# Performance work log

Measured on AMD Instinct MI355X. Metric: run time of the kernel, lower is better.

Reference implementation:

```python
import jax, jax.numpy as jnp
import numpy as np


def _conv(x, kernel):
    # x: [N, C, H, W], kernel: [O, I, kh, kw]; torch conv2d padding=1 (symmetric both dims)
    return jax.lax.conv_general_dilated(
        x, kernel, window_strides=(1, 1), padding=((1, 1), (1, 1)),
        dimension_numbers=("NCHW", "OIHW", "NCHW"))


def setup_inputs() -> dict:
    key = jax.random.key(0)
    k1, k2 = jax.random.split(key)
    shape = (2, 7, 7, 3, 256, 256)  # bs, ah, aw, c, h, w
    infer = jax.random.normal(k1, shape, dtype=jnp.float32)
    ref = jax.random.normal(k2, shape, dtype=jnp.float32)
    return {"infer": infer, "ref": ref}


def reference(infer, ref):
    bs, ah, aw, c, h, w = infer.shape
    x = infer.reshape(bs * ah * aw, c, h, w)
    y = ref.reshape(bs * ah * aw, c, h, w)
    # fixed gradient kernels, identical across all 3x3 in/out channel pairs
    kh = jnp.broadcast_to(
        jnp.array([-0.5, 0.0, 0.5], jnp.float32).reshape(1, 1, 1, 3), (3, 3, 1, 3))
    kv = jnp.broadcast_to(
        jnp.array([-0.5, 0.0, 0.5], jnp.float32).reshape(1, 1, 3, 1), (3, 3, 3, 1))
    # torch padding=1 on a (1,3) kernel -> output (h+2, w); on (3,1) -> (h, w+2)
    loss_h = jnp.mean(jnp.abs(_conv(x, kh) - _conv(y, kh)))
    loss_v = jnp.mean(jnp.abs(_conv(x, kv) - _conv(y, kv)))
    return (loss_h + loss_v) / 2.0
```

## Files before the change

kernel.cpp:

```cpp
#include <hip/hip_runtime.h>


#define W 256
#define NIMG 98
#define CH_STRIDE 65536
#define WAVES_PER_BLK 4
#define NROWS (NIMG * 256)
#define NBLK (NROWS / WAVES_PER_BLK)
#define NXCD 8
#define SCALE (0.25f / 6472704.0f)

struct Row6 { float4 a0, a1, a2, b0, b1, b2; };

__device__ __forceinline__ Row6 issue6(const float* __restrict__ xb,
                                       const float* __restrict__ yb, int ro) {
  Row6 r;
  r.a0 = *(const float4*)(xb + ro);
  r.a1 = *(const float4*)(xb + ro + CH_STRIDE);
  r.a2 = *(const float4*)(xb + ro + 2 * CH_STRIDE);
  r.b0 = *(const float4*)(yb + ro);
  r.b1 = *(const float4*)(yb + ro + CH_STRIDE);
  r.b2 = *(const float4*)(yb + ro + 2 * CH_STRIDE);
  return r;
}

__device__ __forceinline__ float4 combine(const Row6& r, float m) {
  float4 d;
  d.x = m * ((r.a0.x - r.b0.x) + (r.a1.x - r.b1.x) + (r.a2.x - r.b2.x));
  d.y = m * ((r.a0.y - r.b0.y) + (r.a1.y - r.b1.y) + (r.a2.y - r.b2.y));
  d.z = m * ((r.a0.z - r.b0.z) + (r.a1.z - r.b1.z) + (r.a2.z - r.b2.z));
  d.w = m * ((r.a0.w - r.b0.w) + (r.a1.w - r.b1.w) + (r.a2.w - r.b2.w));
  return d;
}

__device__ __forceinline__ float row_task(const float* __restrict__ x,
                                          const float* __restrict__ y,
                                          int task, int lane) {
  const int n = task >> 8;
  const int h = task & 255;

  const float* xb = x + (size_t)n * 3 * CH_STRIDE + (lane << 2);
  const float* yb = y + (size_t)n * 3 * CH_STRIDE + (lane << 2);

  const int hm = (h > 0)   ? h - 1 : 0;
  const int hp = (h < 255) ? h + 1 : 255;

  Row6 rm = issue6(xb, yb, hm * W);
  Row6 rc = issue6(xb, yb, h  * W);
  Row6 rp = issue6(xb, yb, hp * W);

  float4 dm = combine(rm, (h > 0)   ? 1.f : 0.f);
  float4 dc = combine(rc, 1.f);
  float4 dp = combine(rp, (h < 255) ? 1.f : 0.f);

  float lm = __shfl_up(dc.w, 1);
  if (lane == 0) lm = 0.f;
  float rr = __shfl_down(dc.x, 1);
  if (lane == 63) rr = 0.f;
  float acc = fabsf(dc.y - lm) + fabsf(dc.z - dc.x)
            + fabsf(dc.w - dc.y) + fabsf(rr - dc.z);

  acc += fabsf(dp.x - dm.x) + fabsf(dp.y - dm.y)
       + fabsf(dp.z - dm.z) + fabsf(dp.w - dm.w);

  #pragma unroll
  for (int off = 32; off > 0; off >>= 1)
    acc += __shfl_down(acc, off, 64);
  return acc;
}

__device__ __forceinline__ int swz_block(int bid) {
  const int chunk = NBLK / NXCD;
  return (bid % NXCD) * chunk + bid / NXCD;
}

__device__ __forceinline__ float block_body(const float* __restrict__ x,
                                            const float* __restrict__ y) {
  const int tid  = threadIdx.x;
  const int lane = tid & 63;
  const int wv   = tid >> 6;
  const int task = swz_block(blockIdx.x) * WAVES_PER_BLK + wv;

  float s = row_task(x, y, task, lane);

  __shared__ float ws[WAVES_PER_BLK];
  if (lane == 0) ws[wv] = s;
  __syncthreads();
  return ws[0] + ws[1] + ws[2] + ws[3];
}

__global__ __launch_bounds__(256) void detail_stage1(
    const float* __restrict__ x, const float* __restrict__ y,
    float* __restrict__ partial) {
  float s = block_body(x, y);
  if (threadIdx.x == 0) partial[blockIdx.x] = s;
}

__global__ __launch_bounds__(256) void detail_stage1_atomic(
    const float* __restrict__ x, const float* __restrict__ y,
    float* __restrict__ out) {
  float s = block_body(x, y);
  if (threadIdx.x == 0) atomicAdd(out, s * SCALE);
}

__global__ __launch_bounds__(256) void detail_stage2(
    const float* __restrict__ partial, float* __restrict__ out) {
  float acc = 0.f;
  for (int i = threadIdx.x; i < NBLK; i += 256) acc += partial[i];
  #pragma unroll
  for (int off = 32; off > 0; off >>= 1)
    acc += __shfl_down(acc, off, 64);
  __shared__ float ws[4];
  if ((threadIdx.x & 63) == 0) ws[threadIdx.x >> 6] = acc;
  __syncthreads();
  if (threadIdx.x == 0) out[0] = (ws[0] + ws[1] + ws[2] + ws[3]) * SCALE;
}

extern "C" void kernel_launch(void* const* d_in, const int* in_sizes, int n_in,
                              void* d_out, int out_size, void* d_ws, size_t ws_size,
                              hipStream_t stream) {
  const float* infer = (const float*)d_in[0];
  const float* ref   = (const float*)d_in[1];
  float* out = (float*)d_out;

  if (ws_size >= NBLK * sizeof(float)) {
    float* partial = (float*)d_ws;
    detail_stage1<<<NBLK, 256, 0, stream>>>(infer, ref, partial);
    detail_stage2<<<1, 256, 0, stream>>>(partial, out);
  } else {
    hipMemsetAsync(out, 0, sizeof(float), stream);
    detail_stage1_atomic<<<NBLK, 256, 0, stream>>>(infer, ref, out);
  }
}
```

Baseline: 180.5 us.

## Split into channel-difference pass plus stencil pass over materialized D buffer

Adds a first kernel that reduces the six input planes to a single difference image D, written to workspace, and a second kernel where each wave handles a 4-row strip of D, reusing loaded rows across neighbouring stencil rows instead of reloading three rows from six planes per output row. This removes the threefold redundant reads of the inputs that the old one-row-per-wave kernel relied on the cache to absorb. The cost is an extra round trip of D through global memory (about a third of the input size), an additional kernel launch, and the need for a much larger workspace. The old atomic fallback path is kept, but without XCD block swizzling.

```diff
diff --git a/kernel.cpp b/kernel.cpp
--- a/kernel.cpp
+++ b/kernel.cpp
@@ -4,11 +4,99 @@
 #define W 256
 #define NIMG 98
 #define CH_STRIDE 65536
-#define WAVES_PER_BLK 4
-#define NROWS (NIMG * 256)
-#define NBLK (NROWS / WAVES_PER_BLK)
-#define NXCD 8
+#define IMG_F4 16384
+#define TOT_F4 (NIMG * IMG_F4)
+#define P1_BLK (TOT_F4 / 256)
+#define NBAND2 (NIMG * 64)
+#define P2_BLK (NBAND2 / 4)
+#define D_FLOATS (NIMG * 65536)
+#define WS_NEED ((size_t)D_FLOATS * 4 + P2_BLK * 4)
 #define SCALE (0.25f / 6472704.0f)
+
+__global__ __launch_bounds__(256) void compute_d(
+    const float* __restrict__ x, const float* __restrict__ y,
+    float4* __restrict__ D) {
+  const int i = blockIdx.x * 256 + threadIdx.x;
+  const int n = i >> 14;
+  const int e = i & 16383;
+  const float4* xb = (const float4*)x + (size_t)n * 3 * IMG_F4 + e;
+  const float4* yb = (const float4*)y + (size_t)n * 3 * IMG_F4 + e;
+  const float4 a0 = xb[0], a1 = xb[IMG_F4], a2 = xb[2 * IMG_F4];
+  const float4 b0 = yb[0], b1 = yb[IMG_F4], b2 = yb[2 * IMG_F4];
+  float4 d;
+  d.x = (a0.x - b0.x) + (a1.x - b1.x) + (a2.x - b2.x);
+  d.y = (a0.y - b0.y) + (a1.y - b1.y) + (a2.y - b2.y);
+  d.z = (a0.z - b0.z) + (a1.z - b1.z) + (a2.z - b2.z);
+  d.w = (a0.w - b0.w) + (a1.w - b1.w) + (a2.w - b2.w);
+  D[i] = d;
+}
+
+__global__ __launch_bounds__(256) void detail_stencil(
+    const float4* __restrict__ D, float* __restrict__ partial) {
+  const int tid  = threadIdx.x;
+  const int lane = tid & 63;
+  const int wv   = tid >> 6;
+  const int band = blockIdx.x * 4 + wv;
+  const int n     = band >> 6;
+  const int strip = band & 63;
+  const int r0    = strip * 4;
+
+  const float4* Db = D + (size_t)n * IMG_F4 + lane;
+
+  const int gm = (r0 > 0) ? (r0 - 1) : 0;
+  const int gp = (r0 + 4 < 256) ? (r0 + 4) : 255;
+
+  float4 d0 = Db[gm * 64];
+  float4 d1 = Db[r0 * 64];
+  float4 d2 = Db[(r0 + 1) * 64];
+  float4 d3 = Db[(r0 + 2) * 64];
+  float4 d4 = Db[(r0 + 3) * 64];
+  float4 d5 = Db[gp * 64];
+
+  const float m0 = (r0 > 0) ? 1.f : 0.f;
+  const float m5 = (r0 + 4 < 256) ? 1.f : 0.f;
+  d0.x *= m0; d0.y *= m0; d0.z *= m0; d0.w *= m0;
+  d5.x *= m5; d5.y *= m5; d5.z *= m5; d5.w *= m5;
+
+  float acc = 0.f;
+  #define ACCROW(Dm, Dc, Dp) do {                                     \
+    float lm_ = __shfl_up((Dc).w, 1);                                 \
+    if (lane == 0) lm_ = 0.f;                                         \
+    float rr_ = __shfl_down((Dc).x, 1);                               \
+    if (lane == 63) rr_ = 0.f;                                        \
+    acc += fabsf((Dc).y - lm_) + fabsf((Dc).z - (Dc).x)              \
+         + fabsf((Dc).w - (Dc).y) + fabsf(rr_ - (Dc).z);             \
+    acc += fabsf((Dp).x - (Dm).x) + fabsf((Dp).y - (Dm).y)           \
+         + fabsf((Dp).z - (Dm).z) + fabsf((Dp).w - (Dm).w);          \
+  } while (0)
+
+  ACCROW(d0, d1, d2);
+  ACCROW(d1, d2, d3);
+  ACCROW(d2, d3, d4);
+  ACCROW(d3, d4, d5);
+  #undef ACCROW
+
+  #pragma unroll
+  for (int off = 32; off > 0; off >>= 1)
+    acc += __shfl_down(acc, off, 64);
+  __shared__ float ws[4];
+  if (lane == 0) ws[wv] = acc;
+  __syncthreads();
+  if (tid == 0) partial[blockIdx.x] = ws[0] + ws[1] + ws[2] + ws[3];
+}
+
+__global__ __launch_bounds__(256) void detail_stage2(
+    const float* __restrict__ partial, float* __restrict__ out) {
+  float acc = 0.f;
+  for (int i = threadIdx.x; i < P2_BLK; i += 256) acc += partial[i];
+  #pragma unroll
+  for (int off = 32; off > 0; off >>= 1)
+    acc += __shfl_down(acc, off, 64);
+  __shared__ float ws[4];
+  if ((threadIdx.x & 63) == 0) ws[threadIdx.x >> 6] = acc;
+  __syncthreads();
+  if (threadIdx.x == 0) out[0] = (ws[0] + ws[1] + ws[2] + ws[3]) * SCALE;
+}
 
 struct Row6 { float4 a0, a1, a2, b0, b1, b2; };
 
@@ -33,23 +121,25 @@
   return d;
 }
 
-__device__ __forceinline__ float row_task(const float* __restrict__ x,
-                                          const float* __restrict__ y,
-                                          int task, int lane) {
+__global__ __launch_bounds__(256) void detail_atomic(
+    const float* __restrict__ x, const float* __restrict__ y,
+    float* __restrict__ out) {
+  const int tid  = threadIdx.x;
+  const int lane = tid & 63;
+  const int wv   = tid >> 6;
+  const int task = blockIdx.x * 4 + wv;
   const int n = task >> 8;
   const int h = task & 255;
 
   const float* xb = x + (size_t)n * 3 * CH_STRIDE + (lane << 2);
   const float* yb = y + (size_t)n * 3 * CH_STRIDE + (lane << 2);
-
-  const int hm = (h > 0)   ? h - 1 : 0;
+  const int hm = (h > 0) ? h - 1 : 0;
   const int hp = (h < 255) ? h + 1 : 255;
 
   Row6 rm = issue6(xb, yb, hm * W);
-  Row6 rc = issue6(xb, yb, h  * W);
+  Row6 rc = issue6(xb, yb, h * W);
   Row6 rp = issue6(xb, yb, hp * W);
-
-  float4 dm = combine(rm, (h > 0)   ? 1.f : 0.f);
+  float4 dm = combine(rm, (h > 0) ? 1.f : 0.f);
   float4 dc = combine(rc, 1.f);
   float4 dp = combine(rp, (h < 255) ? 1.f : 0.f);
 
@@ -59,61 +149,17 @@
   if (lane == 63) rr = 0.f;
   float acc = fabsf(dc.y - lm) + fabsf(dc.z - dc.x)
             + fabsf(dc.w - dc.y) + fabsf(rr - dc.z);
-
   acc += fabsf(dp.x - dm.x) + fabsf(dp.y - dm.y)
        + fabsf(dp.z - dm.z) + fabsf(dp.w - dm.w);
 
   #pragma unroll
   for (int off = 32; off > 0; off >>= 1)
     acc += __shfl_down(acc, off, 64);
-  return acc;
-}
-
-__device__ __forceinline__ int swz_block(int bid) {
-  const int chunk = NBLK / NXCD;
-  return (bid % NXCD) * chunk + bid / NXCD;
-}
-
-__device__ __forceinline__ float block_body(const float* __restrict__ x,
-                                            const float* __restrict__ y) {
-  const int tid  = threadIdx.x;
-  const int lane = tid & 63;
-  const int wv   = tid >> 6;
-  const int task = swz_block(blockIdx.x) * WAVES_PER_BLK + wv;
-
-  float s = row_task(x, y, task, lane);
-
-  __shared__ float ws[WAVES_PER_BLK];
-  if (lane == 0) ws[wv] = s;
+  __shared__ float ws[4];
+  if (lane == 0) ws[wv] = acc;
   __syncthreads();
-  return ws[0] + ws[1] + ws[2] + ws[3];
-}
-
-__global__ __launch_bounds__(256) void detail_stage1(
-    const float* __restrict__ x, const float* __restrict__ y,
-    float* __restrict__ partial) {
-  float s = block_body(x, y);
-  if (threadIdx.x == 0) partial[blockIdx.x] = s;
-}
-
-__global__ __launch_bounds__(256) void detail_stage1_atomic(
-    const float* __restrict__ x, const float* __restrict__ y,
-    float* __restrict__ out) {
-  float s = block_body(x, y);
-  if (threadIdx.x == 0) atomicAdd(out, s * SCALE);
-}
-
-__global__ __launch_bounds__(256) void detail_stage2(
-    const float* __restrict__ partial, float* __restrict__ out) {
-  float acc = 0.f;
-  for (int i = threadIdx.x; i < NBLK; i += 256) acc += partial[i];
-  #pragma unroll
-  for (int off = 32; off > 0; off >>= 1)
-    acc += __shfl_down(acc, off, 64);
-  __shared__ float ws[4];
-  if ((threadIdx.x & 63) == 0) ws[threadIdx.x >> 6] = acc;
-  __syncthreads();
-  if (threadIdx.x == 0) out[0] = (ws[0] + ws[1] + ws[2] + ws[3]) * SCALE;
+  if (tid == 0)
+    atomicAdd(out, (ws[0] + ws[1] + ws[2] + ws[3]) * SCALE);
 }
 
 extern "C" void kernel_launch(void* const* d_in, const int* in_sizes, int n_in,
@@ -123,12 +169,14 @@
   const float* ref   = (const float*)d_in[1];
   float* out = (float*)d_out;
 
-  if (ws_size >= NBLK * sizeof(float)) {
-    float* partial = (float*)d_ws;
-    detail_stage1<<<NBLK, 256, 0, stream>>>(infer, ref, partial);
+  if (ws_size >= WS_NEED) {
+    float4* D      = (float4*)d_ws;
+    float* partial = (float*)d_ws + D_FLOATS;
+    compute_d<<<P1_BLK, 256, 0, stream>>>(infer, ref, D);
+    detail_stencil<<<P2_BLK, 256, 0, stream>>>(D, partial);
     detail_stage2<<<1, 256, 0, stream>>>(partial, out);
   } else {
     hipMemsetAsync(out, 0, sizeof(float), stream);
-    detail_stage1_atomic<<<NBLK, 256, 0, stream>>>(infer, ref, out);
+    detail_atomic<<<25088 / 4, 256, 0, stream>>>(infer, ref, out);
   }
 }
```

New measurement: 174.3 us. 3.4% less time.
